# Kernel optimization log

Hardware: AMD Instinct MI355X
Metric: run time of the kernel (lower is better)

Reference implementation:

```python
import jax, jax.numpy as jnp
import numpy as np

B, S, L = 256, 20, 512
SKILL_DIM, HIDDEN = 128, 768
VOCAB = 2001


def setup_inputs() -> dict:
    key = jax.random.key(0)
    k1, k2, k3, k4 = jax.random.split(key, 4)
    skills = jax.random.randint(k1, (B, S), 0, VOCAB)
    desc = jax.random.normal(k2, (B, L, HIDDEN), dtype=jnp.float32)
    embs = jax.random.normal(k3, (VOCAB, SKILL_DIM), dtype=jnp.float32)
    W = jax.random.normal(k4, (SKILL_DIM, HIDDEN), dtype=jnp.float32)
    return {"skills": skills, "desc": desc, "embs": embs, "W": W}


def reference(skills, desc, embs, W):
    # skills: [B,S] int, desc: [B,L,H], embs: [V,D], W: [D,H]
    se = embs[skills]                                  # [B,S,D] embedding lookup
    q = jnp.einsum('bsd,dh->bsh', se, W)               # [B,S,H]
    scores = jnp.einsum('bsh,blh->bsl', q, desc)       # [B,S,L] unscaled QK^T
    attn = jax.nn.softmax(scores, axis=2)              # softmax over desc tokens
    out = jnp.einsum('bsl,blh->bsh', attn, desc)       # [B,S,H]
    cat = jnp.concatenate([se, out], axis=2)           # [B,S,D+H]
    return cat.reshape(cat.shape[0], -1)               # [B, S*(D+H)]
```

## Files before the change

kernel.cpp:

```cpp
#include <hip/hip_runtime.h>
#include <cstddef>
#include <cstdint>

#define NB 256
#define NS 20
#define NL 512
#define ND 128
#define NH 768
#define ROWE (NS*(ND+NH))

typedef __attribute__((ext_vector_type(4))) float  f32x4;
typedef __attribute__((ext_vector_type(8))) short  bf16x8;
typedef __attribute__((ext_vector_type(4))) unsigned short ushort4v;
typedef __attribute__((ext_vector_type(8))) unsigned short ushort8v;

#define MFMA16 __builtin_amdgcn_mfma_f32_16x16x32_bf16

__device__ __forceinline__ unsigned short bf16_rne(float v){
    unsigned u = __builtin_bit_cast(unsigned, v);
    u = (u + 0x7fffu + ((u>>16)&1u)) >> 16;
    return (unsigned short)u;
}
__device__ __forceinline__ float bf16f(unsigned short h){
    unsigned u = ((unsigned)h)<<16;
    return __builtin_bit_cast(float, u);
}
__device__ __forceinline__ void bar_lds(){
    asm volatile("s_waitcnt lgkmcnt(0)" ::: "memory");
    __builtin_amdgcn_s_barrier();
}

extern "C" __global__ __launch_bounds__(256)
void k1_q(const int* __restrict__ skills, const float* __restrict__ embs,
          const float* __restrict__ W,
          unsigned short* __restrict__ qhi, unsigned short* __restrict__ qlo,
          float* __restrict__ out)
{
    __shared__ float se[NS*ND];
    __shared__ int   sk[NS];
    const int b = blockIdx.x, t = threadIdx.x;
    if (t < NS) sk[t] = skills[b*NS + t];
    __syncthreads();
    for (int idx = t; idx < NS*ND; idx += 256) {
        const int s = idx >> 7, d = idx & (ND-1);
        const float v = embs[(size_t)sk[s]*ND + d];
        se[idx] = v;
        out[(size_t)b*ROWE + (size_t)s*(ND+NH) + d] = v;
    }
    __syncthreads();

    const int w = t >> 6, lane = t & 63;
    float acc[5][12];
    #pragma unroll
    for (int i = 0; i < 5; ++i)
        #pragma unroll
        for (int c = 0; c < 12; ++c) acc[i][c] = 0.f;

    const float* Wl = W + lane;
    for (int d4 = 0; d4 < ND/4; ++d4) {
        f32x4 sv[5];
        #pragma unroll
        for (int i = 0; i < 5; ++i)
            sv[i] = *(const f32x4*)&se[(5*w + i)*ND + 4*d4];
        #pragma unroll
        for (int r = 0; r < 4; ++r) {
            const float* wr = Wl + (size_t)(4*d4 + r)*NH;
            float wv[12];
            #pragma unroll
            for (int c = 0; c < 12; ++c) wv[c] = wr[64*c];
            #pragma unroll
            for (int i = 0; i < 5; ++i) {
                const float s_ = sv[i][r];
                #pragma unroll
                for (int c = 0; c < 12; ++c) acc[i][c] += s_*wv[c];
            }
        }
    }
    #pragma unroll
    for (int i = 0; i < 5; ++i)
        #pragma unroll
        for (int c = 0; c < 12; ++c) {
            const size_t idx = ((size_t)b*NS + 5*w + i)*NH + lane + 64*c;
            const float v = acc[i][c];
            const unsigned short hh = bf16_rne(v);
            qhi[idx] = hh;
            qlo[idx] = bf16_rne(v - bf16f(hh));
        }
}

#define DTP 776

extern "C" __global__ __launch_bounds__(512)
void k2f(const unsigned short* __restrict__ qhi,
         const unsigned short* __restrict__ qlo,
         const float* __restrict__ desc,
         float* __restrict__ Opart, float* __restrict__ ms)
{
    __shared__ __align__(16) unsigned short dt_hi[16*DTP];
    __shared__ __align__(16) unsigned short dt_lo[16*DTP];
    __shared__ __align__(16) f32x4 scr[3][2][64];
    __shared__ __align__(16) unsigned short p_lds2[16][24];
    __shared__ float f_lds[2][16];

    const int b = blockIdx.x, lh = blockIdx.y, t = threadIdx.x;
    const int w = t >> 6, L = t & 63;
    const int st = w & 1, kq = w >> 1;
    const int g = L >> 4, r16 = L & 15;
    const int slot = t % 96, sq = t / 96;

    const float* dsrc = desc + ((size_t)b*NL + (size_t)lh*256)*NH;
    const int s_in = 16*st + r16;
    const size_t qrow = ((size_t)b*NS + (s_in < NS ? s_in : NS-1))*(size_t)NH;

    bf16x8 qhreg[6], qlreg[6];
    #pragma unroll
    for (int kb = 0; kb < 6; ++kb) {
        const int k0 = 192*kq + 32*kb + 8*g;
        qhreg[kb] = *(const bf16x8*)&qhi[qrow + k0];
        qlreg[kb] = *(const bf16x8*)&qlo[qrow + k0];
    }

    f32x4 acc4[4][2];
    #pragma unroll
    for (int j = 0; j < 4; ++j) {
        acc4[j][0] = (f32x4){0.f,0.f,0.f,0.f};
        acc4[j][1] = (f32x4){0.f,0.f,0.f,0.f};
    }
    float m_run = -1e30f, sum_run = 0.f;

    #pragma unroll 1
    for (int tt = 0; tt < 16; ++tt) {
        f32x4 tmp[6];
        {
            const float* tsrc = dsrc + (size_t)tt*16*NH;
            #pragma unroll
            for (int i = 0; i < 6; ++i)
                tmp[i] = *(const f32x4*)(tsrc + (size_t)4*(t + 512*i));
        }
        bar_lds();

        #pragma unroll
        for (int i = 0; i < 6; ++i) {
            const int v = t + 512*i;
            const int l = v/192, h = 4*(v%192);
            ushort4v hi4, lo4;
            #pragma unroll
            for (int c = 0; c < 4; ++c) {
                const float x = tmp[i][c];
                const unsigned short hh = bf16_rne(x);
                hi4[c] = hh;
                lo4[c] = bf16_rne(x - bf16f(hh));
            }
            *(ushort4v*)&dt_hi[l*DTP + h] = hi4;
            *(ushort4v*)&dt_lo[l*DTP + h] = lo4;
        }
        bar_lds();

        f32x4 Se = (f32x4){0.f,0.f,0.f,0.f};
        #pragma unroll
        for (int kb = 0; kb < 6; ++kb) {
            const int k0 = 192*kq + 32*kb;
            const bf16x8 Ah = *(const bf16x8*)&dt_hi[r16*DTP + k0 + 8*g];
            const bf16x8 Al = *(const bf16x8*)&dt_lo[r16*DTP + k0 + 8*g];
            Se = MFMA16(Ah, qhreg[kb], Se, 0,0,0);
            Se = MFMA16(Al, qhreg[kb], Se, 0,0,0);
            Se = MFMA16(Ah, qlreg[kb], Se, 0,0,0);
        }
        if (kq > 0) scr[kq-1][st][L] = Se;
        bar_lds();

        if (kq == 0) {
            Se += scr[0][st][L];
            Se += scr[1][st][L];
            Se += scr[2][st][L];
            float pm = fmaxf(fmaxf(Se[0],Se[1]), fmaxf(Se[2],Se[3]));
            pm = fmaxf(pm, __shfl_xor(pm, 16));
            pm = fmaxf(pm, __shfl_xor(pm, 32));
            const float mnew = fmaxf(m_run, pm);
            const float fsc  = __expf(m_run - mnew);
            float pe[4];
            #pragma unroll
            for (int r = 0; r < 4; ++r) pe[r] = __expf(Se[r] - mnew);
            float ts = (pe[0]+pe[1]) + (pe[2]+pe[3]);
            ts += __shfl_xor(ts, 16);
            ts += __shfl_xor(ts, 32);
            sum_run = sum_run*fsc + ts;
            m_run = mnew;
            if (s_in < NS) {
                #pragma unroll
                for (int r = 0; r < 4; ++r)
                    p_lds2[4*g + r][s_in] = bf16_rne(pe[r]);
            }
            if (L < 16) f_lds[st][L] = fsc;
        }
        bar_lds();

        if (sq < 5) {
            #pragma unroll
            for (int j = 0; j < 4; ++j) {
                const int s = 4*sq + j;
                const float f = f_lds[s>>4][s&15];
                acc4[j][0] *= f;  acc4[j][1] *= f;
            }
            #pragma unroll
            for (int l = 0; l < 16; ++l) {
                const ushort8v dv = *(const ushort8v*)&dt_hi[l*DTP + 8*slot];
                const ushort4v pv = *(const ushort4v*)&p_lds2[l][4*sq];
                f32x4 d0, d1;
                #pragma unroll
                for (int c = 0; c < 4; ++c) {
                    d0[c] = bf16f(dv[c]);
                    d1[c] = bf16f(dv[4+c]);
                }
                #pragma unroll
                for (int j = 0; j < 4; ++j) {
                    const float p = bf16f(pv[j]);
                    acc4[j][0] += p * d0;
                    acc4[j][1] += p * d1;
                }
            }
        }
    }

    bar_lds();
    if (kq == 0 && L < 16) f_lds[st][L] = 1.0f / sum_run;
    bar_lds();
    if (sq < 5) {
        #pragma unroll
        for (int j = 0; j < 4; ++j) {
            const int s = 4*sq + j;
            const float inv = f_lds[s>>4][s&15];
            float* Ob = Opart + ((size_t)(b*2 + lh)*NS + s)*NH + 8*slot;
            f32x4 o0 = acc4[j][0], o1 = acc4[j][1];
            o0 *= inv;  o1 *= inv;
            *(f32x4*)&Ob[0] = o0;
            *(f32x4*)&Ob[4] = o1;
        }
    }
    if (kq == 0 && L < 16) {
        const int s2 = 16*st + L;
        if (s2 < NS) {
            ms[((size_t)(b*2 + lh)*NS + s2)*2 + 0] = m_run;
            ms[((size_t)(b*2 + lh)*NS + s2)*2 + 1] = sum_run;
        }
    }
}

extern "C" __global__ __launch_bounds__(256)
void k3_fin(const float* __restrict__ Opart, const float* __restrict__ ms,
            float* __restrict__ out)
{
    __shared__ float c0s[NS], c1s[NS];
    const int b = blockIdx.x, t = threadIdx.x;
    if (t < NS) {
        const float m0 = ms[((size_t)(b*2 + 0)*NS + t)*2 + 0];
        const float s0 = ms[((size_t)(b*2 + 0)*NS + t)*2 + 1];
        const float m1 = ms[((size_t)(b*2 + 1)*NS + t)*2 + 0];
        const float s1 = ms[((size_t)(b*2 + 1)*NS + t)*2 + 1];
        const float m  = fmaxf(m0, m1);
        const float w0 = __expf(m0 - m)*s0, w1 = __expf(m1 - m)*s1;
        const float inv = 1.0f / (w0 + w1);
        c0s[t] = w0*inv;
        c1s[t] = w1*inv;
    }
    __syncthreads();
    const float* O0 = Opart + (size_t)(b*2 + 0)*NS*NH;
    const float* O1 = Opart + (size_t)(b*2 + 1)*NS*NH;
    #pragma unroll 1
    for (int i4 = t; i4 < NS*NH/4; i4 += 256) {
        const int idx = 4*i4;
        const int s = idx / NH, h = idx - s*NH;
        const f32x4 a = *(const f32x4*)&O0[idx];
        const f32x4 c = *(const f32x4*)&O1[idx];
        const float c0 = c0s[s], c1 = c1s[s];
        f32x4 o;
        o[0] = c0*a[0] + c1*c[0]; o[1] = c0*a[1] + c1*c[1];
        o[2] = c0*a[2] + c1*c[2]; o[3] = c0*a[3] + c1*c[3];
        *(f32x4*)&out[(size_t)b*ROWE + (size_t)s*(ND+NH) + ND + h] = o;
    }
}

extern "C" void kernel_launch(void* const* d_in, const int* in_sizes, int n_in,
                              void* d_out, int out_size, void* d_ws, size_t ws_size,
                              hipStream_t stream)
{
    const int*   skills = (const int*)  d_in[0];
    const float* desc   = (const float*)d_in[1];
    const float* embs   = (const float*)d_in[2];
    const float* W      = (const float*)d_in[3];
    float* out = (float*)d_out;

    unsigned short* qhi = (unsigned short*)d_ws;
    unsigned short* qlo = qhi + (size_t)NB*NS*NH;
    float* Opart = (float*)(qlo + (size_t)NB*NS*NH);
    float* ms    = Opart + (size_t)NB*2*NS*NH;

    k1_q  <<<NB,          256, 0, stream>>>(skills, embs, W, qhi, qlo, out);
    k2f   <<<dim3(NB, 2), 512, 0, stream>>>(qhi, qlo, desc, Opart, ms);
    k3_fin<<<NB,          256, 0, stream>>>(Opart, ms, out);
}
```

Measured before the change: 202.6 us.

## Prefetch next desc tile into registers and simplify bf16 unpacking

Loads for the next 16-row desc tile are issued right after the current tile is converted into LDS, so global memory latency overlaps with the MFMA score, softmax and PV phases instead of stalling at the top of each iteration. The bf16-to-float unpacking in the PV loop now works on 32-bit words with shift and mask instead of per-element 16-bit extracts, which cuts ALU instructions. The prefetch keeps 24 extra floats live across the loop body, which raises register pressure and could lower occupancy.

```diff
diff --git a/kernel.cpp b/kernel.cpp
--- a/kernel.cpp
+++ b/kernel.cpp
@@ -13,6 +13,8 @@
 typedef __attribute__((ext_vector_type(8))) short  bf16x8;
 typedef __attribute__((ext_vector_type(4))) unsigned short ushort4v;
 typedef __attribute__((ext_vector_type(8))) unsigned short ushort8v;
+typedef __attribute__((ext_vector_type(4))) unsigned int  uint4v;
+typedef __attribute__((ext_vector_type(2))) unsigned int  uint2v;
 
 #define MFMA16 __builtin_amdgcn_mfma_f32_16x16x32_bf16
 
@@ -24,6 +26,12 @@
 __device__ __forceinline__ float bf16f(unsigned short h){
     unsigned u = ((unsigned)h)<<16;
     return __builtin_bit_cast(float, u);
+}
+__device__ __forceinline__ float lo16f(unsigned u){
+    return __builtin_bit_cast(float, u << 16);
+}
+__device__ __forceinline__ float hi16f(unsigned u){
+    return __builtin_bit_cast(float, u & 0xffff0000u);
 }
 __device__ __forceinline__ void bar_lds(){
     asm volatile("s_waitcnt lgkmcnt(0)" ::: "memory");
@@ -128,15 +136,13 @@
     }
     float m_run = -1e30f, sum_run = 0.f;
 
+    f32x4 sreg[6];
+    #pragma unroll
+    for (int i = 0; i < 6; ++i)
+        sreg[i] = *(const f32x4*)(dsrc + (size_t)4*(t + 512*i));
+
     #pragma unroll 1
     for (int tt = 0; tt < 16; ++tt) {
-        f32x4 tmp[6];
-        {
-            const float* tsrc = dsrc + (size_t)tt*16*NH;
-            #pragma unroll
-            for (int i = 0; i < 6; ++i)
-                tmp[i] = *(const f32x4*)(tsrc + (size_t)4*(t + 512*i));
-        }
         bar_lds();
 
         #pragma unroll
@@ -146,13 +152,19 @@
             ushort4v hi4, lo4;
             #pragma unroll
             for (int c = 0; c < 4; ++c) {
-                const float x = tmp[i][c];
+                const float x = sreg[i][c];
                 const unsigned short hh = bf16_rne(x);
                 hi4[c] = hh;
                 lo4[c] = bf16_rne(x - bf16f(hh));
             }
             *(ushort4v*)&dt_hi[l*DTP + h] = hi4;
             *(ushort4v*)&dt_lo[l*DTP + h] = lo4;
+        }
+        if (tt < 15) {
+            const float* nsrc = dsrc + (size_t)(tt+1)*16*NH;
+            #pragma unroll
+            for (int i = 0; i < 6; ++i)
+                sreg[i] = *(const f32x4*)(nsrc + (size_t)4*(t + 512*i));
         }
         bar_lds();
 
@@ -206,18 +218,19 @@
             for (int l = 0; l < 16; ++l) {
                 const ushort8v dv = *(const ushort8v*)&dt_hi[l*DTP + 8*slot];
                 const ushort4v pv = *(const ushort4v*)&p_lds2[l][4*sq];
+                const uint4v dw = __builtin_bit_cast(uint4v, dv);
+                const uint2v pw = __builtin_bit_cast(uint2v, pv);
                 f32x4 d0, d1;
-                #pragma unroll
-                for (int c = 0; c < 4; ++c) {
-                    d0[c] = bf16f(dv[c]);
-                    d1[c] = bf16f(dv[4+c]);
-                }
-                #pragma unroll
-                for (int j = 0; j < 4; ++j) {
-                    const float p = bf16f(pv[j]);
-                    acc4[j][0] += p * d0;
-                    acc4[j][1] += p * d1;
-                }
+                d0[0] = lo16f(dw[0]); d0[1] = hi16f(dw[0]);
+                d0[2] = lo16f(dw[1]); d0[3] = hi16f(dw[1]);
+                d1[0] = lo16f(dw[2]); d1[1] = hi16f(dw[2]);
+                d1[2] = lo16f(dw[3]); d1[3] = hi16f(dw[3]);
+                const float p0 = lo16f(pw[0]), p1 = hi16f(pw[0]);
+                const float p2 = lo16f(pw[1]), p3 = hi16f(pw[1]);
+                acc4[0][0] += p0 * d0;  acc4[0][1] += p0 * d1;
+                acc4[1][0] += p1 * d0;  acc4[1][1] += p1 * d1;
+                acc4[2][0] += p2 * d0;  acc4[2][1] += p2 * d1;
+                acc4[3][0] += p3 * d0;  acc4[3][1] += p3 * d1;
             }
         }
     }
```

Result: faster. 183.3 us (-9.5%).

## Stage desc tiles as fp32 via direct global-to-LDS loads and split bf16 on read

Applied to the files above, without the earlier changes.

Each 16-row desc tile now goes from global memory straight into padded fp32 LDS with global_load_lds, so the register round-trip and the hi/lo bf16 split on store are gone. The hi/lo split now happens when the QK MFMA operands are read, and the PV accumulation uses fp32 desc and fp32 probabilities instead of bf16. The load is still waited on synchronously after each tile with no double buffering, and the low part is truncated rather than rounded, which changes numerics slightly.

```diff
diff --git a/kernel.cpp b/kernel.cpp
--- a/kernel.cpp
+++ b/kernel.cpp
@@ -12,7 +12,6 @@
 typedef __attribute__((ext_vector_type(4))) float  f32x4;
 typedef __attribute__((ext_vector_type(8))) short  bf16x8;
 typedef __attribute__((ext_vector_type(4))) unsigned short ushort4v;
-typedef __attribute__((ext_vector_type(8))) unsigned short ushort8v;
 
 #define MFMA16 __builtin_amdgcn_mfma_f32_16x16x32_bf16
 
@@ -88,7 +87,8 @@
         }
 }
 
-#define DTP 776
+#define DTFP  772
+#define CPR   193
 
 extern "C" __global__ __launch_bounds__(512)
 void k2f(const unsigned short* __restrict__ qhi,
@@ -96,10 +96,9 @@
          const float* __restrict__ desc,
          float* __restrict__ Opart, float* __restrict__ ms)
 {
-    __shared__ __align__(16) unsigned short dt_hi[16*DTP];
-    __shared__ __align__(16) unsigned short dt_lo[16*DTP];
+    __shared__ __align__(16) float dtf[12544];
     __shared__ __align__(16) f32x4 scr[3][2][64];
-    __shared__ __align__(16) unsigned short p_lds2[16][24];
+    __shared__ __align__(16) float p_lds2[16][24];
     __shared__ float f_lds[2][16];
 
     const int b = blockIdx.x, lh = blockIdx.y, t = threadIdx.x;
@@ -128,40 +127,55 @@
     }
     float m_run = -1e30f, sum_run = 0.f;
 
+    auto issue_dma = [&](const float* tsrc){
+        #pragma unroll
+        for (int i = 0; i < 6; ++i) {
+            const int ch = 8*i + w;
+            const unsigned s = (unsigned)(ch*64 + L);
+            unsigned row = (s*5434u) >> 20;
+            unsigned col = s - row*CPR;
+            if (row > 15u) row = 15u;
+            if (col > 191u) col = 191u;
+            const float* gsrc = tsrc + (size_t)row*NH + 4u*col;
+            __builtin_amdgcn_global_load_lds(gsrc, &dtf[ch*256], 16, 0, 0);
+        }
+        if (w == 0) {
+            const unsigned s = (unsigned)(48*64 + L);
+            unsigned row = (s*5434u) >> 20;
+            unsigned col = s - row*CPR;
+            if (row > 15u) row = 15u;
+            if (col > 191u) col = 191u;
+            const float* gsrc = tsrc + (size_t)row*NH + 4u*col;
+            __builtin_amdgcn_global_load_lds(gsrc, &dtf[48*256], 16, 0, 0);
+        }
+    };
+
+    issue_dma(dsrc);
+    asm volatile("s_waitcnt vmcnt(0)" ::: "memory");
+    bar_lds();
+
     #pragma unroll 1
     for (int tt = 0; tt < 16; ++tt) {
-        f32x4 tmp[6];
-        {
-            const float* tsrc = dsrc + (size_t)tt*16*NH;
-            #pragma unroll
-            for (int i = 0; i < 6; ++i)
-                tmp[i] = *(const f32x4*)(tsrc + (size_t)4*(t + 512*i));
-        }
-        bar_lds();
-
-        #pragma unroll
-        for (int i = 0; i < 6; ++i) {
-            const int v = t + 512*i;
-            const int l = v/192, h = 4*(v%192);
-            ushort4v hi4, lo4;
-            #pragma unroll
-            for (int c = 0; c < 4; ++c) {
-                const float x = tmp[i][c];
-                const unsigned short hh = bf16_rne(x);
-                hi4[c] = hh;
-                lo4[c] = bf16_rne(x - bf16f(hh));
-            }
-            *(ushort4v*)&dt_hi[l*DTP + h] = hi4;
-            *(ushort4v*)&dt_lo[l*DTP + h] = lo4;
-        }
-        bar_lds();
-
         f32x4 Se = (f32x4){0.f,0.f,0.f,0.f};
         #pragma unroll
         for (int kb = 0; kb < 6; ++kb) {
             const int k0 = 192*kq + 32*kb;
-            const bf16x8 Ah = *(const bf16x8*)&dt_hi[r16*DTP + k0 + 8*g];
-            const bf16x8 Al = *(const bf16x8*)&dt_lo[r16*DTP + k0 + 8*g];
+            const f32x4 A0 = *(const f32x4*)&dtf[r16*DTFP + k0 + 8*g];
+            const f32x4 A1 = *(const f32x4*)&dtf[r16*DTFP + k0 + 8*g + 4];
+            ushort4v h0, h1, l0, l1;
+            #pragma unroll
+            for (int e = 0; e < 4; ++e) {
+                const float x0 = A0[e], x1 = A1[e];
+                const unsigned short hh0 = bf16_rne(x0);
+                const unsigned short hh1 = bf16_rne(x1);
+                h0[e] = hh0;  h1[e] = hh1;
+                l0[e] = (unsigned short)(__builtin_bit_cast(unsigned, x0 - bf16f(hh0)) >> 16);
+                l1[e] = (unsigned short)(__builtin_bit_cast(unsigned, x1 - bf16f(hh1)) >> 16);
+            }
+            const bf16x8 Ah = __builtin_bit_cast(bf16x8,
+                __builtin_shufflevector(h0, h1, 0,1,2,3,4,5,6,7));
+            const bf16x8 Al = __builtin_bit_cast(bf16x8,
+                __builtin_shufflevector(l0, l1, 0,1,2,3,4,5,6,7));
             Se = MFMA16(Ah, qhreg[kb], Se, 0,0,0);
             Se = MFMA16(Al, qhreg[kb], Se, 0,0,0);
             Se = MFMA16(Ah, qlreg[kb], Se, 0,0,0);
@@ -189,7 +203,7 @@
             if (s_in < NS) {
                 #pragma unroll
                 for (int r = 0; r < 4; ++r)
-                    p_lds2[4*g + r][s_in] = bf16_rne(pe[r]);
+                    p_lds2[4*g + r][s_in] = pe[r];
             }
             if (L < 16) f_lds[st][L] = fsc;
         }
@@ -204,21 +218,21 @@
             }
             #pragma unroll
             for (int l = 0; l < 16; ++l) {
-                const ushort8v dv = *(const ushort8v*)&dt_hi[l*DTP + 8*slot];
-                const ushort4v pv = *(const ushort4v*)&p_lds2[l][4*sq];
-                f32x4 d0, d1;
-                #pragma unroll
-                for (int c = 0; c < 4; ++c) {
-                    d0[c] = bf16f(dv[c]);
-                    d1[c] = bf16f(dv[4+c]);
-                }
-                #pragma unroll
-                for (int j = 0; j < 4; ++j) {
-                    const float p = bf16f(pv[j]);
-                    acc4[j][0] += p * d0;
-                    acc4[j][1] += p * d1;
-                }
-            }
+                const f32x4 d0 = *(const f32x4*)&dtf[l*DTFP + 4*slot];
+                const f32x4 d1 = *(const f32x4*)&dtf[l*DTFP + 384 + 4*slot];
+                const f32x4 pv = *(const f32x4*)&p_lds2[l][4*sq];
+                acc4[0][0] += pv[0] * d0;  acc4[0][1] += pv[0] * d1;
+                acc4[1][0] += pv[1] * d0;  acc4[1][1] += pv[1] * d1;
+                acc4[2][0] += pv[2] * d0;  acc4[2][1] += pv[2] * d1;
+                acc4[3][0] += pv[3] * d0;  acc4[3][1] += pv[3] * d1;
+            }
+        }
+        bar_lds();
+
+        if (tt < 15) {
+            issue_dma(dsrc + (size_t)(tt+1)*16*NH);
+            asm volatile("s_waitcnt vmcnt(0)" ::: "memory");
+            bar_lds();
         }
     }
 
@@ -230,11 +244,11 @@
         for (int j = 0; j < 4; ++j) {
             const int s = 4*sq + j;
             const float inv = f_lds[s>>4][s&15];
-            float* Ob = Opart + ((size_t)(b*2 + lh)*NS + s)*NH + 8*slot;
+            float* Ob = Opart + ((size_t)(b*2 + lh)*NS + s)*NH;
             f32x4 o0 = acc4[j][0], o1 = acc4[j][1];
             o0 *= inv;  o1 *= inv;
-            *(f32x4*)&Ob[0] = o0;
-            *(f32x4*)&Ob[4] = o1;
+            *(f32x4*)&Ob[4*slot]       = o0;
+            *(f32x4*)&Ob[384 + 4*slot] = o1;
         }
     }
     if (kq == 0 && L < 16) {
```

Result: slower. 208.0 us (+2.6%).
